# Performance work log

Measured on AMD Instinct MI355X. Metric: run time of the kernel, lower is better.

The kernel has to match this reference:

```python
import jax, jax.numpy as jnp
import numpy as np

T, H, I, E, K = 8192, 1024, 2048, 8, 2


def setup_inputs() -> dict:
    key = jax.random.key(0)
    ks = jax.random.split(key, 6)
    s_h = 1.0 / np.sqrt(H)
    s_i = 1.0 / np.sqrt(I)
    return {
        "x": jax.random.normal(ks[0], (T, H), dtype=jnp.float32),
        "Wr": jax.random.normal(ks[1], (H, E), dtype=jnp.float32) * s_h,
        "br": jnp.zeros((E,), dtype=jnp.float32),
        "Wg": jax.random.normal(ks[2], (E, H, I), dtype=jnp.float32) * s_h,
        "Wu": jax.random.normal(ks[3], (E, H, I), dtype=jnp.float32) * s_h,
        "Wd": jax.random.normal(ks[4], (E, I, H), dtype=jnp.float32) * s_i,
    }


def reference(x, Wr, br, Wg, Wu, Wd):
    # Router: dense GEMM + top-k + sigmoid gate renormalization
    logits = x @ Wr + br                            # [T, E]
    topk_vals, topk_idx = jax.lax.top_k(logits, K)  # [T, K]
    g = jax.nn.sigmoid(topk_vals)
    g = g / (jnp.sum(g, axis=-1, keepdims=True) + 1e-10)
    # Scatter gates to dense [T, E] combine weights (zero for unselected experts)
    gates = jnp.zeros((x.shape[0], Wr.shape[1]), dtype=x.dtype)
    gates = gates.at[jnp.arange(x.shape[0])[:, None], topk_idx].add(g)
    # SwiGLU expert MLP, computed densely over experts and combined by gates
    h_gate = jnp.einsum("th,ehi->tei", x, Wg)       # [T, E, I]
    h_up = jnp.einsum("th,ehi->tei", x, Wu)
    h = jax.nn.silu(h_gate) * h_up
    h = h * gates[:, :, None]                       # fuse gate combine before down-proj
    out = jnp.einsum("tei,eih->th", h, Wd)          # [T, H]
    return out
```

## Files before the change

kernel.cpp:

```cpp
#include <hip/hip_runtime.h>
#include <hip/hip_bf16.h>
#include <stdint.h>

#define TT 8192
#define HH 1024
#define II 2048
#define EE 8
#define TOPK 2

typedef __bf16 bf16x8 __attribute__((ext_vector_type(8)));
typedef float f32x4 __attribute__((ext_vector_type(4)));

__device__ __forceinline__ unsigned short f2bf(float f) {
  union { float f; unsigned int u; } c; c.f = f;
  unsigned int u = c.u;
  u += 0x7FFFu + ((u >> 16) & 1u);
  return (unsigned short)(u >> 16);
}

__device__ __forceinline__ void gload_lds16(const void* g, void* l) {
  __builtin_amdgcn_global_load_lds((const __attribute__((address_space(1))) void*)g,
                                   (__attribute__((address_space(3))) void*)l, 16, 0, 0);
}

__global__ __launch_bounds__(256) void k_convert_x(const float4* __restrict__ src,
                                                   ushort4* __restrict__ dst, int n4) {
  int i = blockIdx.x * 256 + threadIdx.x;
  if (i >= n4) return;
  float4 v = src[i];
  ushort4 o;
  o.x = f2bf(v.x); o.y = f2bf(v.y); o.z = f2bf(v.z); o.w = f2bf(v.w);
  dst[i] = o;
}

__global__ __launch_bounds__(256) void k_transpose_cvt(const float* __restrict__ src,
                                                       unsigned short* __restrict__ dst,
                                                       int R, int C) {
  __shared__ float tile[64][65];
  const float* s = src + (size_t)blockIdx.z * R * C;
  unsigned short* d = dst + (size_t)blockIdx.z * R * C;
  int r0 = blockIdx.y * 64, c0 = blockIdx.x * 64;
  int tx = threadIdx.x & 15;
  int ty = threadIdx.x >> 4;
#pragma unroll
  for (int i = 0; i < 4; ++i) {
    int rr = i * 16 + ty;
    float4 v = *reinterpret_cast<const float4*>(&s[(size_t)(r0 + rr) * C + c0 + tx * 4]);
    tile[rr][tx * 4 + 0] = v.x; tile[rr][tx * 4 + 1] = v.y;
    tile[rr][tx * 4 + 2] = v.z; tile[rr][tx * 4 + 3] = v.w;
  }
  __syncthreads();
#pragma unroll
  for (int i = 0; i < 4; ++i) {
    int cc = i * 16 + ty;
    ushort4 o;
    o.x = f2bf(tile[tx * 4 + 0][cc]);
    o.y = f2bf(tile[tx * 4 + 1][cc]);
    o.z = f2bf(tile[tx * 4 + 2][cc]);
    o.w = f2bf(tile[tx * 4 + 3][cc]);
    *reinterpret_cast<ushort4*>(&d[(size_t)(c0 + cc) * R + r0 + tx * 4]) = o;
  }
}

__global__ __launch_bounds__(256) void k_router(const float* __restrict__ x,
                                                const float* __restrict__ Wr,
                                                const float* __restrict__ br,
                                                int* __restrict__ tlist,
                                                float* __restrict__ glist,
                                                int* __restrict__ counts) {
  __shared__ float wrt[8][1024];
  __shared__ int lcount[8];
  __shared__ int lbase[8];
  __shared__ short ent_e[128];
  __shared__ short ent_slot[128];
  __shared__ float ent_g[128];
  int tid = threadIdx.x;
  for (int i = tid; i < 8192; i += 256) {
    wrt[i & 7][i >> 3] = Wr[i];
  }
  if (tid < 8) lcount[tid] = 0;
  __syncthreads();
  int w = tid >> 6, l = tid & 63;
  int t0 = blockIdx.x * 64;
  for (int it = 0; it < 16; ++it) {
    int t = t0 + w * 16 + it;
    const float4* xr = reinterpret_cast<const float4*>(x + (size_t)t * HH);
    float acc[8] = {0.f, 0.f, 0.f, 0.f, 0.f, 0.f, 0.f, 0.f};
#pragma unroll
    for (int j = 0; j < 4; ++j) {
      float4 xv = xr[j * 64 + l];
      int hbase = (j * 64 + l) * 4;
#pragma unroll
      for (int e = 0; e < 8; ++e) {
        float4 wv = *reinterpret_cast<const float4*>(&wrt[e][hbase]);
        acc[e] += xv.x * wv.x + xv.y * wv.y + xv.z * wv.z + xv.w * wv.w;
      }
    }
#pragma unroll
    for (int e = 0; e < 8; ++e)
#pragma unroll
      for (int off = 32; off > 0; off >>= 1) acc[e] += __shfl_xor(acc[e], off, 64);
    if (l == 0) {
      float lg[8];
#pragma unroll
      for (int e = 0; e < 8; ++e) lg[e] = acc[e] + br[e];
      int i0 = 0;
#pragma unroll
      for (int e = 1; e < 8; ++e) if (lg[e] > lg[i0]) i0 = e;
      int i1 = (i0 == 0) ? 1 : 0;
#pragma unroll
      for (int e = 0; e < 8; ++e) if (e != i0 && lg[e] > lg[i1]) i1 = e;
      float g0 = 1.f / (1.f + expf(-lg[i0]));
      float g1 = 1.f / (1.f + expf(-lg[i1]));
      float inv = 1.f / (g0 + g1 + 1e-10f);
      int idx = (w * 16 + it) * 2;
      int s0 = atomicAdd(&lcount[i0], 1);
      ent_e[idx] = (short)i0; ent_slot[idx] = (short)s0; ent_g[idx] = g0 * inv;
      int s1 = atomicAdd(&lcount[i1], 1);
      ent_e[idx + 1] = (short)i1; ent_slot[idx + 1] = (short)s1; ent_g[idx + 1] = g1 * inv;
    }
  }
  __syncthreads();
  if (tid < 8) lbase[tid] = atomicAdd(&counts[tid], lcount[tid]);
  __syncthreads();
  if (tid < 128) {
    int e = ent_e[tid];
    int slot = lbase[e] + ent_slot[tid];
    int t = t0 + (tid >> 1);
    tlist[e * TT + slot] = t;
    glist[e * TT + slot] = ent_g[tid];
  }
}

__global__ void k_offsets(const int* __restrict__ counts, int* __restrict__ offs) {
  if (threadIdx.x == 0) {
    int s = 0;
    for (int e = 0; e < EE; ++e) { offs[e] = s; s += counts[e]; }
  }
}

__global__ __launch_bounds__(256, 2) void k_gemm1(
    const unsigned short* __restrict__ xb,
    const unsigned short* __restrict__ WgT,
    const unsigned short* __restrict__ WuT,
    const int* __restrict__ tlist, const float* __restrict__ glist,
    const int* __restrict__ counts, const int* __restrict__ offs,
    unsigned short* __restrict__ hbuf) {
  __shared__ unsigned short lsA[128 * 64];
  __shared__ unsigned short lsG[128 * 64];
  __shared__ unsigned short lsU[128 * 64];
  __shared__ int s_tok[128];
  __shared__ float s_gate[128];

  const int e = blockIdx.z;
  const int n_e = counts[e];
  const int row0 = blockIdx.y * 128;
  if (row0 >= n_e) return;
  const int n0 = blockIdx.x * 128;
  const int tid = threadIdx.x;

  if (tid < 128) {
    int r = row0 + tid;
    int tok = 0; float gt = 0.f;
    if (r < n_e) { tok = tlist[e * TT + r]; gt = glist[e * TT + r]; }
    s_tok[tid] = tok; s_gate[tid] = gt;
  }
  __syncthreads();

  const int scol = (tid & 7) ^ ((tid >> 3) & 7);
  const unsigned short* srcA[4];
  const unsigned short* srcG[4];
  const unsigned short* srcU[4];
#pragma unroll
  for (int i = 0; i < 4; ++i) {
    int row = i * 32 + (tid >> 3);
    srcA[i] = xb + (size_t)s_tok[row] * HH + scol * 8;
    size_t wrow = ((size_t)e * II + n0 + row) * HH + scol * 8;
    srcG[i] = WgT + wrow;
    srcU[i] = WuT + wrow;
  }

  f32x4 zero = {0.f, 0.f, 0.f, 0.f};
  f32x4 accg[4][4], accu[4][4];
#pragma unroll
  for (int m = 0; m < 4; ++m)
#pragma unroll
    for (int n = 0; n < 4; ++n) { accg[m][n] = zero; accu[m][n] = zero; }

  const int l = tid & 63;
  const int w = tid >> 6;
  const int wr = (w >> 1) * 64;
  const int wc = (w & 1) * 64;
  const int lrow = l & 15;
  const int lk = l >> 4;
  const int swz = (l & 7) << 4;
  const int aoff0 = (wr + lrow) * 128 + lk * 16;
  const int boff0 = (wc + lrow) * 128 + lk * 16;
  const char* lcA = (const char*)lsA;
  const char* lcG = (const char*)lsG;
  const char* lcU = (const char*)lsU;

  for (int kt = 0; kt < HH / 64; ++kt) {
#pragma unroll
    for (int i = 0; i < 4; ++i) {
      gload_lds16(srcA[i] + kt * 64, (char*)lsA + i * 4096 + tid * 16);
      gload_lds16(srcG[i] + kt * 64, (char*)lsG + i * 4096 + tid * 16);
      gload_lds16(srcU[i] + kt * 64, (char*)lsU + i * 4096 + tid * 16);
    }
    __syncthreads();
#pragma unroll
    for (int kk = 0; kk < 2; ++kk) {
      bf16x8 af[4], bg[4], bu[4];
#pragma unroll
      for (int m = 0; m < 4; ++m)
        af[m] = *(const bf16x8*)(lcA + ((aoff0 + m * 2048 + kk * 64) ^ swz));
#pragma unroll
      for (int n = 0; n < 4; ++n) {
        bg[n] = *(const bf16x8*)(lcG + ((boff0 + n * 2048 + kk * 64) ^ swz));
        bu[n] = *(const bf16x8*)(lcU + ((boff0 + n * 2048 + kk * 64) ^ swz));
      }
#pragma unroll
      for (int m = 0; m < 4; ++m)
#pragma unroll
        for (int n = 0; n < 4; ++n) {
          accg[m][n] = __builtin_amdgcn_mfma_f32_16x16x32_bf16(af[m], bg[n], accg[m][n], 0, 0, 0);
          accu[m][n] = __builtin_amdgcn_mfma_f32_16x16x32_bf16(af[m], bu[n], accu[m][n], 0, 0, 0);
        }
    }
    __syncthreads();
  }

  const int obase = offs[e];
#pragma unroll
  for (int m = 0; m < 4; ++m)
#pragma unroll
    for (int n = 0; n < 4; ++n)
#pragma unroll
      for (int r = 0; r < 4; ++r) {
        int rl = wr + m * 16 + lk * 4 + r;
        if (row0 + rl < n_e) {
          float gv = accg[m][n][r];
          float uv = accu[m][n][r];
          float val = gv / (1.f + __expf(-gv)) * uv * s_gate[rl];
          hbuf[(size_t)(obase + row0 + rl) * II + n0 + wc + n * 16 + lrow] = f2bf(val);
        }
      }
}

__global__ __launch_bounds__(256, 2) void k_gemm2(
    const unsigned short* __restrict__ hbuf,
    const unsigned short* __restrict__ WdT,
    const int* __restrict__ tlist,
    const int* __restrict__ counts, const int* __restrict__ offs,
    float* __restrict__ out) {
  __shared__ unsigned short lsA[128 * 64];
  __shared__ unsigned short lsB[128 * 64];
  __shared__ int s_tok[128];

  const int e = blockIdx.z;
  const int n_e = counts[e];
  const int row0 = blockIdx.y * 128;
  if (row0 >= n_e) return;
  const int n0 = blockIdx.x * 128;
  const int tid = threadIdx.x;
  const int obase = offs[e];

  if (tid < 128) {
    int r = row0 + tid;
    s_tok[tid] = (r < n_e) ? tlist[e * TT + r] : 0;
  }
  __syncthreads();

  const int scol = (tid & 7) ^ ((tid >> 3) & 7);
  const unsigned short* srcA[4];
  const unsigned short* srcB[4];
#pragma unroll
  for (int i = 0; i < 4; ++i) {
    int row = i * 32 + (tid >> 3);
    int ar = obase + row0 + row;
    if (ar > TT * TOPK - 1) ar = TT * TOPK - 1;
    srcA[i] = hbuf + (size_t)ar * II + scol * 8;
    srcB[i] = WdT + ((size_t)e * HH + n0 + row) * II + scol * 8;
  }

  f32x4 zero = {0.f, 0.f, 0.f, 0.f};
  f32x4 acc[4][4];
#pragma unroll
  for (int m = 0; m < 4; ++m)
#pragma unroll
    for (int n = 0; n < 4; ++n) acc[m][n] = zero;

  const int l = tid & 63;
  const int w = tid >> 6;
  const int wr = (w >> 1) * 64;
  const int wc = (w & 1) * 64;
  const int lrow = l & 15;
  const int lk = l >> 4;
  const int swz = (l & 7) << 4;
  const int aoff0 = (wr + lrow) * 128 + lk * 16;
  const int boff0 = (wc + lrow) * 128 + lk * 16;
  const char* lcA = (const char*)lsA;
  const char* lcB = (const char*)lsB;

  for (int kt = 0; kt < II / 64; ++kt) {
#pragma unroll
    for (int i = 0; i < 4; ++i) {
      gload_lds16(srcA[i] + kt * 64, (char*)lsA + i * 4096 + tid * 16);
      gload_lds16(srcB[i] + kt * 64, (char*)lsB + i * 4096 + tid * 16);
    }
    __syncthreads();
#pragma unroll
    for (int kk = 0; kk < 2; ++kk) {
      bf16x8 af[4], bf[4];
#pragma unroll
      for (int m = 0; m < 4; ++m)
        af[m] = *(const bf16x8*)(lcA + ((aoff0 + m * 2048 + kk * 64) ^ swz));
#pragma unroll
      for (int n = 0; n < 4; ++n)
        bf[n] = *(const bf16x8*)(lcB + ((boff0 + n * 2048 + kk * 64) ^ swz));
#pragma unroll
      for (int m = 0; m < 4; ++m)
#pragma unroll
        for (int n = 0; n < 4; ++n)
          acc[m][n] = __builtin_amdgcn_mfma_f32_16x16x32_bf16(af[m], bf[n], acc[m][n], 0, 0, 0);
    }
    __syncthreads();
  }

#pragma unroll
  for (int m = 0; m < 4; ++m)
#pragma unroll
    for (int n = 0; n < 4; ++n)
#pragma unroll
      for (int r = 0; r < 4; ++r) {
        int rl = wr + m * 16 + lk * 4 + r;
        if (row0 + rl < n_e) {
          int t = s_tok[rl];
          unsafeAtomicAdd(&out[(size_t)t * HH + n0 + wc + n * 16 + lrow], acc[m][n][r]);
        }
      }
}

extern "C" void kernel_launch(void* const* d_in, const int* in_sizes, int n_in,
                              void* d_out, int out_size, void* d_ws, size_t ws_size,
                              hipStream_t stream) {
  const float* x  = (const float*)d_in[0];
  const float* Wr = (const float*)d_in[1];
  const float* br = (const float*)d_in[2];
  const float* Wg = (const float*)d_in[3];
  const float* Wu = (const float*)d_in[4];
  const float* Wd = (const float*)d_in[5];
  float* out = (float*)d_out;

  char* ws = (char*)d_ws;
  size_t off = 0;
  auto alloc = [&](size_t bytes) {
    char* p = ws + off;
    off += (bytes + 255) & ~(size_t)255;
    return p;
  };
  unsigned short* xb   = (unsigned short*)alloc((size_t)TT * HH * 2);
  unsigned short* WgT  = (unsigned short*)alloc((size_t)EE * HH * II * 2);
  unsigned short* WuT  = (unsigned short*)alloc((size_t)EE * HH * II * 2);
  unsigned short* WdT  = (unsigned short*)alloc((size_t)EE * HH * II * 2);
  unsigned short* hbuf = (unsigned short*)alloc((size_t)TT * TOPK * II * 2);
  int*   tlist  = (int*)alloc((size_t)EE * TT * 4);
  float* glist  = (float*)alloc((size_t)EE * TT * 4);
  int*   counts = (int*)alloc(128);
  int*   offs   = (int*)alloc(128);

  hipMemsetAsync(counts, 0, 128, stream);
  hipMemsetAsync(d_out, 0, (size_t)TT * HH * 4, stream);

  k_convert_x<<<(TT * HH / 4 + 255) / 256, 256, 0, stream>>>(
      (const float4*)x, (ushort4*)xb, TT * HH / 4);

  dim3 tg1(II / 64, HH / 64, EE);
  k_transpose_cvt<<<tg1, 256, 0, stream>>>(Wg, WgT, HH, II);
  k_transpose_cvt<<<tg1, 256, 0, stream>>>(Wu, WuT, HH, II);
  dim3 tg2(HH / 64, II / 64, EE);
  k_transpose_cvt<<<tg2, 256, 0, stream>>>(Wd, WdT, II, HH);

  k_router<<<TT / 64, 256, 0, stream>>>(x, Wr, br, tlist, glist, counts);
  k_offsets<<<1, 64, 0, stream>>>(counts, offs);

  dim3 g1(II / 128, TT / 128, EE);
  k_gemm1<<<g1, 256, 0, stream>>>(xb, WgT, WuT, tlist, glist, counts, offs, hbuf);
  dim3 g2(HH / 128, TT / 128, EE);
  k_gemm2<<<g2, 256, 0, stream>>>(hbuf, WdT, tlist, counts, offs, out);

  (void)in_sizes; (void)n_in; (void)out_size; (void)ws_size;
}
```

Baseline: 430.8 us.

## Double-buffer gate/up GEMM with 256x128 tiles and fuse x conversion into router

The gate/up expert GEMM now uses 512-thread blocks with a 256x128 output tile. It double-buffers its LDS stages so the global-to-LDS loads for the next k-step overlap the MFMAs of the current one. Hand-placed waitcnt, barriers and setprio replace the plain syncthreads. Separately, the bf16 conversion of x moves into the router kernel, which already reads x, removing one launch and one full pass over x. The larger LDS footprint (about 128KB) limits occupancy to one block per CU, and the final prefetch reads one step past the K range.

```diff
diff --git a/kernel.cpp b/kernel.cpp
--- a/kernel.cpp
+++ b/kernel.cpp
@@ -21,16 +21,6 @@
 __device__ __forceinline__ void gload_lds16(const void* g, void* l) {
   __builtin_amdgcn_global_load_lds((const __attribute__((address_space(1))) void*)g,
                                    (__attribute__((address_space(3))) void*)l, 16, 0, 0);
-}
-
-__global__ __launch_bounds__(256) void k_convert_x(const float4* __restrict__ src,
-                                                   ushort4* __restrict__ dst, int n4) {
-  int i = blockIdx.x * 256 + threadIdx.x;
-  if (i >= n4) return;
-  float4 v = src[i];
-  ushort4 o;
-  o.x = f2bf(v.x); o.y = f2bf(v.y); o.z = f2bf(v.z); o.w = f2bf(v.w);
-  dst[i] = o;
 }
 
 __global__ __launch_bounds__(256) void k_transpose_cvt(const float* __restrict__ src,
@@ -65,6 +55,7 @@
 __global__ __launch_bounds__(256) void k_router(const float* __restrict__ x,
                                                 const float* __restrict__ Wr,
                                                 const float* __restrict__ br,
+                                                unsigned short* __restrict__ xb,
                                                 int* __restrict__ tlist,
                                                 float* __restrict__ glist,
                                                 int* __restrict__ counts) {
@@ -90,6 +81,9 @@
     for (int j = 0; j < 4; ++j) {
       float4 xv = xr[j * 64 + l];
       int hbase = (j * 64 + l) * 4;
+      ushort4 o;
+      o.x = f2bf(xv.x); o.y = f2bf(xv.y); o.z = f2bf(xv.z); o.w = f2bf(xv.w);
+      *reinterpret_cast<ushort4*>(xb + (size_t)t * HH + hbase) = o;
 #pragma unroll
       for (int e = 0; e < 8; ++e) {
         float4 wv = *reinterpret_cast<const float4*>(&wrt[e][hbase]);
@@ -139,27 +133,27 @@
   }
 }
 
-__global__ __launch_bounds__(256, 2) void k_gemm1(
+__global__ __launch_bounds__(512, 2) void k_gemm1(
     const unsigned short* __restrict__ xb,
     const unsigned short* __restrict__ WgT,
     const unsigned short* __restrict__ WuT,
     const int* __restrict__ tlist, const float* __restrict__ glist,
     const int* __restrict__ counts, const int* __restrict__ offs,
     unsigned short* __restrict__ hbuf) {
-  __shared__ unsigned short lsA[128 * 64];
-  __shared__ unsigned short lsG[128 * 64];
-  __shared__ unsigned short lsU[128 * 64];
-  __shared__ int s_tok[128];
-  __shared__ float s_gate[128];
+  __shared__ unsigned short lsA[2][256 * 64];
+  __shared__ unsigned short lsG[2][128 * 64];
+  __shared__ unsigned short lsU[2][128 * 64];
+  __shared__ int s_tok[256];
+  __shared__ float s_gate[256];
 
   const int e = blockIdx.z;
   const int n_e = counts[e];
-  const int row0 = blockIdx.y * 128;
+  const int row0 = blockIdx.y * 256;
   if (row0 >= n_e) return;
   const int n0 = blockIdx.x * 128;
   const int tid = threadIdx.x;
 
-  if (tid < 128) {
+  if (tid < 256) {
     int r = row0 + tid;
     int tok = 0; float gt = 0.f;
     if (r < n_e) { tok = tlist[e * TT + r]; gt = glist[e * TT + r]; }
@@ -169,72 +163,100 @@
 
   const int scol = (tid & 7) ^ ((tid >> 3) & 7);
   const unsigned short* srcA[4];
-  const unsigned short* srcG[4];
-  const unsigned short* srcU[4];
-#pragma unroll
-  for (int i = 0; i < 4; ++i) {
-    int row = i * 32 + (tid >> 3);
-    srcA[i] = xb + (size_t)s_tok[row] * HH + scol * 8;
+  const unsigned short* srcG[2];
+  const unsigned short* srcU[2];
+#pragma unroll
+  for (int j = 0; j < 4; ++j) {
+    int row = j * 64 + (tid >> 3);
+    srcA[j] = xb + (size_t)s_tok[row] * HH + scol * 8;
+  }
+#pragma unroll
+  for (int j = 0; j < 2; ++j) {
+    int row = j * 64 + (tid >> 3);
     size_t wrow = ((size_t)e * II + n0 + row) * HH + scol * 8;
-    srcG[i] = WgT + wrow;
-    srcU[i] = WuT + wrow;
-  }
+    srcG[j] = WgT + wrow;
+    srcU[j] = WuT + wrow;
+  }
+
+  auto STAGE = [&](int buf, int koff) {
+    char* dA = (char*)(&lsA[buf][0]);
+    char* dG = (char*)(&lsG[buf][0]);
+    char* dU = (char*)(&lsU[buf][0]);
+#pragma unroll
+    for (int j = 0; j < 4; ++j)
+      gload_lds16(srcA[j] + koff, dA + j * 8192 + tid * 16);
+#pragma unroll
+    for (int j = 0; j < 2; ++j) {
+      gload_lds16(srcG[j] + koff, dG + j * 8192 + tid * 16);
+      gload_lds16(srcU[j] + koff, dU + j * 8192 + tid * 16);
+    }
+  };
 
   f32x4 zero = {0.f, 0.f, 0.f, 0.f};
-  f32x4 accg[4][4], accu[4][4];
-#pragma unroll
-  for (int m = 0; m < 4; ++m)
-#pragma unroll
-    for (int n = 0; n < 4; ++n) { accg[m][n] = zero; accu[m][n] = zero; }
+  f32x4 accg[8][2], accu[8][2];
+#pragma unroll
+  for (int m = 0; m < 8; ++m)
+#pragma unroll
+    for (int n = 0; n < 2; ++n) { accg[m][n] = zero; accu[m][n] = zero; }
 
   const int l = tid & 63;
   const int w = tid >> 6;
-  const int wr = (w >> 1) * 64;
-  const int wc = (w & 1) * 64;
+  const int wr = (w >> 2) * 128;
+  const int wc = (w & 3) * 32;
   const int lrow = l & 15;
   const int lk = l >> 4;
   const int swz = (l & 7) << 4;
-  const int aoff0 = (wr + lrow) * 128 + lk * 16;
-  const int boff0 = (wc + lrow) * 128 + lk * 16;
-  const char* lcA = (const char*)lsA;
-  const char* lcG = (const char*)lsG;
-  const char* lcU = (const char*)lsU;
-
-  for (int kt = 0; kt < HH / 64; ++kt) {
-#pragma unroll
-    for (int i = 0; i < 4; ++i) {
-      gload_lds16(srcA[i] + kt * 64, (char*)lsA + i * 4096 + tid * 16);
-      gload_lds16(srcG[i] + kt * 64, (char*)lsG + i * 4096 + tid * 16);
-      gload_lds16(srcU[i] + kt * 64, (char*)lsU + i * 4096 + tid * 16);
-    }
-    __syncthreads();
+
+  STAGE(0, 0);
+
+#pragma unroll 1
+  for (int k = 0; k < HH / 64; ++k) {
+    STAGE((k + 1) & 1, (k + 1) * 64);
+    asm volatile("s_waitcnt vmcnt(8)" ::: "memory");
+    __builtin_amdgcn_sched_barrier(0);
+    __builtin_amdgcn_s_barrier();
+    __builtin_amdgcn_sched_barrier(0);
+
+    const char* lcA = (const char*)(&lsA[k & 1][0]);
+    const char* lcG = (const char*)(&lsG[k & 1][0]);
+    const char* lcU = (const char*)(&lsU[k & 1][0]);
 #pragma unroll
     for (int kk = 0; kk < 2; ++kk) {
-      bf16x8 af[4], bg[4], bu[4];
-#pragma unroll
-      for (int m = 0; m < 4; ++m)
-        af[m] = *(const bf16x8*)(lcA + ((aoff0 + m * 2048 + kk * 64) ^ swz));
-#pragma unroll
-      for (int n = 0; n < 4; ++n) {
-        bg[n] = *(const bf16x8*)(lcG + ((boff0 + n * 2048 + kk * 64) ^ swz));
-        bu[n] = *(const bf16x8*)(lcU + ((boff0 + n * 2048 + kk * 64) ^ swz));
+      bf16x8 af[8], bg[2], bu[2];
+#pragma unroll
+      for (int m = 0; m < 8; ++m) {
+        int row = wr + m * 16 + lrow;
+        af[m] = *(const bf16x8*)(lcA + ((row * 128 + kk * 64 + lk * 16) ^ swz));
       }
 #pragma unroll
-      for (int m = 0; m < 4; ++m)
-#pragma unroll
-        for (int n = 0; n < 4; ++n) {
+      for (int n = 0; n < 2; ++n) {
+        int row = wc + n * 16 + lrow;
+        bg[n] = *(const bf16x8*)(lcG + ((row * 128 + kk * 64 + lk * 16) ^ swz));
+        bu[n] = *(const bf16x8*)(lcU + ((row * 128 + kk * 64 + lk * 16) ^ swz));
+      }
+      asm volatile("s_waitcnt lgkmcnt(0)" ::: "memory");
+      __builtin_amdgcn_sched_barrier(0);
+      __builtin_amdgcn_s_setprio(1);
+#pragma unroll
+      for (int m = 0; m < 8; ++m)
+#pragma unroll
+        for (int n = 0; n < 2; ++n) {
           accg[m][n] = __builtin_amdgcn_mfma_f32_16x16x32_bf16(af[m], bg[n], accg[m][n], 0, 0, 0);
           accu[m][n] = __builtin_amdgcn_mfma_f32_16x16x32_bf16(af[m], bu[n], accu[m][n], 0, 0, 0);
         }
-    }
-    __syncthreads();
-  }
+      __builtin_amdgcn_s_setprio(0);
+    }
+    __builtin_amdgcn_sched_barrier(0);
+    __builtin_amdgcn_s_barrier();
+    __builtin_amdgcn_sched_barrier(0);
+  }
+  asm volatile("s_waitcnt vmcnt(0)" ::: "memory");
 
   const int obase = offs[e];
 #pragma unroll
-  for (int m = 0; m < 4; ++m)
-#pragma unroll
-    for (int n = 0; n < 4; ++n)
+  for (int m = 0; m < 8; ++m)
+#pragma unroll
+    for (int n = 0; n < 2; ++n)
 #pragma unroll
       for (int r = 0; r < 4; ++r) {
         int rl = wr + m * 16 + lk * 4 + r;
@@ -372,20 +394,17 @@
   hipMemsetAsync(counts, 0, 128, stream);
   hipMemsetAsync(d_out, 0, (size_t)TT * HH * 4, stream);
 
-  k_convert_x<<<(TT * HH / 4 + 255) / 256, 256, 0, stream>>>(
-      (const float4*)x, (ushort4*)xb, TT * HH / 4);
-
   dim3 tg1(II / 64, HH / 64, EE);
   k_transpose_cvt<<<tg1, 256, 0, stream>>>(Wg, WgT, HH, II);
   k_transpose_cvt<<<tg1, 256, 0, stream>>>(Wu, WuT, HH, II);
   dim3 tg2(HH / 64, II / 64, EE);
   k_transpose_cvt<<<tg2, 256, 0, stream>>>(Wd, WdT, II, HH);
 
-  k_router<<<TT / 64, 256, 0, stream>>>(x, Wr, br, tlist, glist, counts);
+  k_router<<<TT / 64, 256, 0, stream>>>(x, Wr, br, xb, tlist, glist, counts);
   k_offsets<<<1, 64, 0, stream>>>(counts, offs);
 
-  dim3 g1(II / 128, TT / 128, EE);
-  k_gemm1<<<g1, 256, 0, stream>>>(xb, WgT, WuT, tlist, glist, counts, offs, hbuf);
+  dim3 g1(II / 128, 32, EE);
+  k_gemm1<<<g1, 512, 0, stream>>>(xb, WgT, WuT, tlist, glist, counts, offs, hbuf);
   dim3 g2(HH / 128, TT / 128, EE);
   k_gemm2<<<g2, 256, 0, stream>>>(hbuf, WdT, tlist, counts, offs, out);
 
```

Result: slower. 440.9 us (+2.3%).

## Interleave gate/up weights into one matrix, fuse x conversion into router

Applied to the files above, without the earlier changes.

Gate and up weights are transposed into one interleaved [2I, H] layout in 16-row groups, so k_gemm1 runs a single 128x128 GEMM whose adjacent column tiles are the gate/up pairs for the SwiGLU epilogue. This halves LDS use and accumulator registers per block and doubles the grid, and launch bounds rise to 4 blocks per SM for both GEMMs to raise occupancy. The x-to-bf16 conversion now happens inside the router, which already reads x, removing one kernel launch and one full pass over x. The trade-off is that each A tile is now loaded twice, once per gate/up tile pair, and tighter launch bounds risk register spills.

```diff
diff --git a/kernel.cpp b/kernel.cpp
--- a/kernel.cpp
+++ b/kernel.cpp
@@ -21,16 +21,6 @@
 __device__ __forceinline__ void gload_lds16(const void* g, void* l) {
   __builtin_amdgcn_global_load_lds((const __attribute__((address_space(1))) void*)g,
                                    (__attribute__((address_space(3))) void*)l, 16, 0, 0);
-}
-
-__global__ __launch_bounds__(256) void k_convert_x(const float4* __restrict__ src,
-                                                   ushort4* __restrict__ dst, int n4) {
-  int i = blockIdx.x * 256 + threadIdx.x;
-  if (i >= n4) return;
-  float4 v = src[i];
-  ushort4 o;
-  o.x = f2bf(v.x); o.y = f2bf(v.y); o.z = f2bf(v.z); o.w = f2bf(v.w);
-  dst[i] = o;
 }
 
 __global__ __launch_bounds__(256) void k_transpose_cvt(const float* __restrict__ src,
@@ -62,9 +52,40 @@
   }
 }
 
+__global__ __launch_bounds__(256) void k_transpose_wgu(const float* __restrict__ src,
+                                                       unsigned short* __restrict__ dst,
+                                                       int mat) {
+  __shared__ float tile[64][65];
+  const float* s = src + (size_t)blockIdx.z * HH * II;
+  unsigned short* d = dst + (size_t)blockIdx.z * 2 * II * HH;
+  int r0 = blockIdx.y * 64, c0 = blockIdx.x * 64;
+  int tx = threadIdx.x & 15;
+  int ty = threadIdx.x >> 4;
+#pragma unroll
+  for (int i = 0; i < 4; ++i) {
+    int rr = i * 16 + ty;
+    float4 v = *reinterpret_cast<const float4*>(&s[(size_t)(r0 + rr) * II + c0 + tx * 4]);
+    tile[rr][tx * 4 + 0] = v.x; tile[rr][tx * 4 + 1] = v.y;
+    tile[rr][tx * 4 + 2] = v.z; tile[rr][tx * 4 + 3] = v.w;
+  }
+  __syncthreads();
+#pragma unroll
+  for (int i = 0; i < 4; ++i) {
+    int cc = i * 16 + ty;
+    int srow = c0 * 2 + ((cc >> 4) << 5) + mat * 16 + (cc & 15);
+    ushort4 o;
+    o.x = f2bf(tile[tx * 4 + 0][cc]);
+    o.y = f2bf(tile[tx * 4 + 1][cc]);
+    o.z = f2bf(tile[tx * 4 + 2][cc]);
+    o.w = f2bf(tile[tx * 4 + 3][cc]);
+    *reinterpret_cast<ushort4*>(&d[(size_t)srow * HH + r0 + tx * 4]) = o;
+  }
+}
+
 __global__ __launch_bounds__(256) void k_router(const float* __restrict__ x,
                                                 const float* __restrict__ Wr,
                                                 const float* __restrict__ br,
+                                                unsigned short* __restrict__ xb,
                                                 int* __restrict__ tlist,
                                                 float* __restrict__ glist,
                                                 int* __restrict__ counts) {
@@ -90,6 +111,9 @@
     for (int j = 0; j < 4; ++j) {
       float4 xv = xr[j * 64 + l];
       int hbase = (j * 64 + l) * 4;
+      ushort4 o;
+      o.x = f2bf(xv.x); o.y = f2bf(xv.y); o.z = f2bf(xv.z); o.w = f2bf(xv.w);
+      *reinterpret_cast<ushort4*>(xb + (size_t)t * HH + hbase) = o;
 #pragma unroll
       for (int e = 0; e < 8; ++e) {
         float4 wv = *reinterpret_cast<const float4*>(&wrt[e][hbase]);
@@ -139,16 +163,14 @@
   }
 }
 
-__global__ __launch_bounds__(256, 2) void k_gemm1(
+__global__ __launch_bounds__(256, 4) void k_gemm1(
     const unsigned short* __restrict__ xb,
-    const unsigned short* __restrict__ WgT,
-    const unsigned short* __restrict__ WuT,
+    const unsigned short* __restrict__ WguT,
     const int* __restrict__ tlist, const float* __restrict__ glist,
     const int* __restrict__ counts, const int* __restrict__ offs,
     unsigned short* __restrict__ hbuf) {
   __shared__ unsigned short lsA[128 * 64];
-  __shared__ unsigned short lsG[128 * 64];
-  __shared__ unsigned short lsU[128 * 64];
+  __shared__ unsigned short lsB[128 * 64];
   __shared__ int s_tok[128];
   __shared__ float s_gate[128];
 
@@ -169,118 +191,12 @@
 
   const int scol = (tid & 7) ^ ((tid >> 3) & 7);
   const unsigned short* srcA[4];
-  const unsigned short* srcG[4];
-  const unsigned short* srcU[4];
+  const unsigned short* srcB[4];
 #pragma unroll
   for (int i = 0; i < 4; ++i) {
     int row = i * 32 + (tid >> 3);
     srcA[i] = xb + (size_t)s_tok[row] * HH + scol * 8;
-    size_t wrow = ((size_t)e * II + n0 + row) * HH + scol * 8;
-    srcG[i] = WgT + wrow;
-    srcU[i] = WuT + wrow;
-  }
-
-  f32x4 zero = {0.f, 0.f, 0.f, 0.f};
-  f32x4 accg[4][4], accu[4][4];
-#pragma unroll
-  for (int m = 0; m < 4; ++m)
-#pragma unroll
-    for (int n = 0; n < 4; ++n) { accg[m][n] = zero; accu[m][n] = zero; }
-
-  const int l = tid & 63;
-  const int w = tid >> 6;
-  const int wr = (w >> 1) * 64;
-  const int wc = (w & 1) * 64;
-  const int lrow = l & 15;
-  const int lk = l >> 4;
-  const int swz = (l & 7) << 4;
-  const int aoff0 = (wr + lrow) * 128 + lk * 16;
-  const int boff0 = (wc + lrow) * 128 + lk * 16;
-  const char* lcA = (const char*)lsA;
-  const char* lcG = (const char*)lsG;
-  const char* lcU = (const char*)lsU;
-
-  for (int kt = 0; kt < HH / 64; ++kt) {
-#pragma unroll
-    for (int i = 0; i < 4; ++i) {
-      gload_lds16(srcA[i] + kt * 64, (char*)lsA + i * 4096 + tid * 16);
-      gload_lds16(srcG[i] + kt * 64, (char*)lsG + i * 4096 + tid * 16);
-      gload_lds16(srcU[i] + kt * 64, (char*)lsU + i * 4096 + tid * 16);
-    }
-    __syncthreads();
-#pragma unroll
-    for (int kk = 0; kk < 2; ++kk) {
-      bf16x8 af[4], bg[4], bu[4];
-#pragma unroll
-      for (int m = 0; m < 4; ++m)
-        af[m] = *(const bf16x8*)(lcA + ((aoff0 + m * 2048 + kk * 64) ^ swz));
-#pragma unroll
-      for (int n = 0; n < 4; ++n) {
-        bg[n] = *(const bf16x8*)(lcG + ((boff0 + n * 2048 + kk * 64) ^ swz));
-        bu[n] = *(const bf16x8*)(lcU + ((boff0 + n * 2048 + kk * 64) ^ swz));
-      }
-#pragma unroll
-      for (int m = 0; m < 4; ++m)
-#pragma unroll
-        for (int n = 0; n < 4; ++n) {
-          accg[m][n] = __builtin_amdgcn_mfma_f32_16x16x32_bf16(af[m], bg[n], accg[m][n], 0, 0, 0);
-          accu[m][n] = __builtin_amdgcn_mfma_f32_16x16x32_bf16(af[m], bu[n], accu[m][n], 0, 0, 0);
-        }
-    }
-    __syncthreads();
-  }
-
-  const int obase = offs[e];
-#pragma unroll
-  for (int m = 0; m < 4; ++m)
-#pragma unroll
-    for (int n = 0; n < 4; ++n)
-#pragma unroll
-      for (int r = 0; r < 4; ++r) {
-        int rl = wr + m * 16 + lk * 4 + r;
-        if (row0 + rl < n_e) {
-          float gv = accg[m][n][r];
-          float uv = accu[m][n][r];
-          float val = gv / (1.f + __expf(-gv)) * uv * s_gate[rl];
-          hbuf[(size_t)(obase + row0 + rl) * II + n0 + wc + n * 16 + lrow] = f2bf(val);
-        }
-      }
-}
-
-__global__ __launch_bounds__(256, 2) void k_gemm2(
-    const unsigned short* __restrict__ hbuf,
-    const unsigned short* __restrict__ WdT,
-    const int* __restrict__ tlist,
-    const int* __restrict__ counts, const int* __restrict__ offs,
-    float* __restrict__ out) {
-  __shared__ unsigned short lsA[128 * 64];
-  __shared__ unsigned short lsB[128 * 64];
-  __shared__ int s_tok[128];
-
-  const int e = blockIdx.z;
-  const int n_e = counts[e];
-  const int row0 = blockIdx.y * 128;
-  if (row0 >= n_e) return;
-  const int n0 = blockIdx.x * 128;
-  const int tid = threadIdx.x;
-  const int obase = offs[e];
-
-  if (tid < 128) {
-    int r = row0 + tid;
-    s_tok[tid] = (r < n_e) ? tlist[e * TT + r] : 0;
-  }
-  __syncthreads();
-
-  const int scol = (tid & 7) ^ ((tid >> 3) & 7);
-  const unsigned short* srcA[4];
-  const unsigned short* srcB[4];
-#pragma unroll
-  for (int i = 0; i < 4; ++i) {
-    int row = i * 32 + (tid >> 3);
-    int ar = obase + row0 + row;
-    if (ar > TT * TOPK - 1) ar = TT * TOPK - 1;
-    srcA[i] = hbuf + (size_t)ar * II + scol * 8;
-    srcB[i] = WdT + ((size_t)e * HH + n0 + row) * II + scol * 8;
+    srcB[i] = WguT + ((size_t)e * 2 * II + n0 + row) * HH + scol * 8;
   }
 
   f32x4 zero = {0.f, 0.f, 0.f, 0.f};
@@ -302,6 +218,104 @@
   const char* lcA = (const char*)lsA;
   const char* lcB = (const char*)lsB;
 
+  for (int kt = 0; kt < HH / 64; ++kt) {
+#pragma unroll
+    for (int i = 0; i < 4; ++i) {
+      gload_lds16(srcA[i] + kt * 64, (char*)lsA + i * 4096 + tid * 16);
+      gload_lds16(srcB[i] + kt * 64, (char*)lsB + i * 4096 + tid * 16);
+    }
+    __syncthreads();
+#pragma unroll
+    for (int kk = 0; kk < 2; ++kk) {
+      bf16x8 af[4], bf[4];
+#pragma unroll
+      for (int m = 0; m < 4; ++m)
+        af[m] = *(const bf16x8*)(lcA + ((aoff0 + m * 2048 + kk * 64) ^ swz));
+#pragma unroll
+      for (int n = 0; n < 4; ++n)
+        bf[n] = *(const bf16x8*)(lcB + ((boff0 + n * 2048 + kk * 64) ^ swz));
+#pragma unroll
+      for (int m = 0; m < 4; ++m)
+#pragma unroll
+        for (int n = 0; n < 4; ++n)
+          acc[m][n] = __builtin_amdgcn_mfma_f32_16x16x32_bf16(af[m], bf[n], acc[m][n], 0, 0, 0);
+    }
+    __syncthreads();
+  }
+
+  const int obase = offs[e];
+#pragma unroll
+  for (int m = 0; m < 4; ++m)
+#pragma unroll
+    for (int n = 0; n < 4; n += 2)
+#pragma unroll
+      for (int r = 0; r < 4; ++r) {
+        int rl = wr + m * 16 + lk * 4 + r;
+        if (row0 + rl < n_e) {
+          float gv = acc[m][n][r];
+          float uv = acc[m][n + 1][r];
+          float val = gv / (1.f + __expf(-gv)) * uv * s_gate[rl];
+          int L = (n0 >> 1) + (wc >> 1) + (n >> 1) * 16 + lrow;
+          hbuf[(size_t)(obase + row0 + rl) * II + L] = f2bf(val);
+        }
+      }
+}
+
+__global__ __launch_bounds__(256, 4) void k_gemm2(
+    const unsigned short* __restrict__ hbuf,
+    const unsigned short* __restrict__ WdT,
+    const int* __restrict__ tlist,
+    const int* __restrict__ counts, const int* __restrict__ offs,
+    float* __restrict__ out) {
+  __shared__ unsigned short lsA[128 * 64];
+  __shared__ unsigned short lsB[128 * 64];
+  __shared__ int s_tok[128];
+
+  const int e = blockIdx.z;
+  const int n_e = counts[e];
+  const int row0 = blockIdx.y * 128;
+  if (row0 >= n_e) return;
+  const int n0 = blockIdx.x * 128;
+  const int tid = threadIdx.x;
+  const int obase = offs[e];
+
+  if (tid < 128) {
+    int r = row0 + tid;
+    s_tok[tid] = (r < n_e) ? tlist[e * TT + r] : 0;
+  }
+  __syncthreads();
+
+  const int scol = (tid & 7) ^ ((tid >> 3) & 7);
+  const unsigned short* srcA[4];
+  const unsigned short* srcB[4];
+#pragma unroll
+  for (int i = 0; i < 4; ++i) {
+    int row = i * 32 + (tid >> 3);
+    int ar = obase + row0 + row;
+    if (ar > TT * TOPK - 1) ar = TT * TOPK - 1;
+    srcA[i] = hbuf + (size_t)ar * II + scol * 8;
+    srcB[i] = WdT + ((size_t)e * HH + n0 + row) * II + scol * 8;
+  }
+
+  f32x4 zero = {0.f, 0.f, 0.f, 0.f};
+  f32x4 acc[4][4];
+#pragma unroll
+  for (int m = 0; m < 4; ++m)
+#pragma unroll
+    for (int n = 0; n < 4; ++n) acc[m][n] = zero;
+
+  const int l = tid & 63;
+  const int w = tid >> 6;
+  const int wr = (w >> 1) * 64;
+  const int wc = (w & 1) * 64;
+  const int lrow = l & 15;
+  const int lk = l >> 4;
+  const int swz = (l & 7) << 4;
+  const int aoff0 = (wr + lrow) * 128 + lk * 16;
+  const int boff0 = (wc + lrow) * 128 + lk * 16;
+  const char* lcA = (const char*)lsA;
+  const char* lcB = (const char*)lsB;
+
   for (int kt = 0; kt < II / 64; ++kt) {
 #pragma unroll
     for (int i = 0; i < 4; ++i) {
@@ -360,8 +374,7 @@
     return p;
   };
   unsigned short* xb   = (unsigned short*)alloc((size_t)TT * HH * 2);
-  unsigned short* WgT  = (unsigned short*)alloc((size_t)EE * HH * II * 2);
-  unsigned short* WuT  = (unsigned short*)alloc((size_t)EE * HH * II * 2);
+  unsigned short* WguT = (unsigned short*)alloc((size_t)EE * 2 * II * HH * 2);
   unsigned short* WdT  = (unsigned short*)alloc((size_t)EE * HH * II * 2);
   unsigned short* hbuf = (unsigned short*)alloc((size_t)TT * TOPK * II * 2);
   int*   tlist  = (int*)alloc((size_t)EE * TT * 4);
@@ -372,20 +385,17 @@
   hipMemsetAsync(counts, 0, 128, stream);
   hipMemsetAsync(d_out, 0, (size_t)TT * HH * 4, stream);
 
-  k_convert_x<<<(TT * HH / 4 + 255) / 256, 256, 0, stream>>>(
-      (const float4*)x, (ushort4*)xb, TT * HH / 4);
-
-  dim3 tg1(II / 64, HH / 64, EE);
-  k_transpose_cvt<<<tg1, 256, 0, stream>>>(Wg, WgT, HH, II);
-  k_transpose_cvt<<<tg1, 256, 0, stream>>>(Wu, WuT, HH, II);
+  dim3 tgu(II / 64, HH / 64, EE);
+  k_transpose_wgu<<<tgu, 256, 0, stream>>>(Wg, WguT, 0);
+  k_transpose_wgu<<<tgu, 256, 0, stream>>>(Wu, WguT, 1);
   dim3 tg2(HH / 64, II / 64, EE);
   k_transpose_cvt<<<tg2, 256, 0, stream>>>(Wd, WdT, II, HH);
 
-  k_router<<<TT / 64, 256, 0, stream>>>(x, Wr, br, tlist, glist, counts);
+  k_router<<<TT / 64, 256, 0, stream>>>(x, Wr, br, xb, tlist, glist, counts);
   k_offsets<<<1, 64, 0, stream>>>(counts, offs);
 
-  dim3 g1(II / 128, TT / 128, EE);
-  k_gemm1<<<g1, 256, 0, stream>>>(xb, WgT, WuT, tlist, glist, counts, offs, hbuf);
+  dim3 g1(2 * II / 128, TT / 128, EE);
+  k_gemm1<<<g1, 256, 0, stream>>>(xb, WguT, tlist, glist, counts, offs, hbuf);
   dim3 g2(HH / 128, TT / 128, EE);
   k_gemm2<<<g2, 256, 0, stream>>>(hbuf, WdT, tlist, counts, offs, out);
 
```

After: 390.7 us. 1.1x faster.
